# Kernel optimization log

Measured on AMD Instinct MI355X. Metric: run time of the kernel, lower is better.

The kernel has to match this reference:

```python
import jax, jax.numpy as jnp
import numpy as np

N_NODES = 10000
N_EDGES = 320000
IN_DIM = 64
HIDDEN = 128
HEADS = 4
OUT_DIM = 64
NEG_SLOPE = 0.2  # PyG GATConv default leaky_relu slope


def setup_inputs() -> dict:
    key = jax.random.key(0)
    ks = jax.random.split(key, 20)
    s = 0.05
    inp = {
        "x": jax.random.normal(ks[0], (N_NODES, IN_DIM), jnp.float32),
        "edge_index": jax.random.randint(ks[1], (2, N_EDGES), 0, N_NODES, jnp.int64),
        # GRU layer 0 (input IN_DIM -> HIDDEN), gates ordered [r, z, n] as in torch
        "w_ih0": jax.random.normal(ks[2], (3 * HIDDEN, IN_DIM), jnp.float32) * s,
        "w_hh0": jax.random.normal(ks[3], (3 * HIDDEN, HIDDEN), jnp.float32) * s,
        "b_ih0": jax.random.normal(ks[4], (3 * HIDDEN,), jnp.float32) * s,
        "b_hh0": jax.random.normal(ks[5], (3 * HIDDEN,), jnp.float32) * s,
        # GRU layer 1 (HIDDEN -> HIDDEN)
        "w_ih1": jax.random.normal(ks[6], (3 * HIDDEN, HIDDEN), jnp.float32) * s,
        "w_hh1": jax.random.normal(ks[7], (3 * HIDDEN, HIDDEN), jnp.float32) * s,
        "b_ih1": jax.random.normal(ks[8], (3 * HIDDEN,), jnp.float32) * s,
        "b_hh1": jax.random.normal(ks[9], (3 * HIDDEN,), jnp.float32) * s,
        # GAT layer 1: HIDDEN -> HIDDEN per head, HEADS heads, concat
        "W1": jax.random.normal(ks[10], (HIDDEN, HEADS * HIDDEN), jnp.float32) * s,
        "att_src1": jax.random.normal(ks[11], (HEADS, HIDDEN), jnp.float32) * s,
        "att_dst1": jax.random.normal(ks[12], (HEADS, HIDDEN), jnp.float32) * s,
        "bias1": jnp.zeros((HEADS * HIDDEN,), jnp.float32),
        # GAT layer 2: HEADS*HIDDEN -> OUT_DIM, 1 head
        "W2": jax.random.normal(ks[13], (HEADS * HIDDEN, OUT_DIM), jnp.float32) * s,
        "att_src2": jax.random.normal(ks[14], (1, OUT_DIM), jnp.float32) * s,
        "att_dst2": jax.random.normal(ks[15], (1, OUT_DIM), jnp.float32) * s,
        "bias2": jnp.zeros((OUT_DIM,), jnp.float32),
    }
    return inp


def _gru_layer(x, w_ih, w_hh, b_ih, b_hh):
    # x: [T, in]; torch GRU cell, unbatched, gates [r, z, n]
    H = w_hh.shape[1]
    gi = x @ w_ih.T + b_ih  # [T, 3H] precomputed input projections

    def step(h, gi_t):
        gh = h @ w_hh.T + b_hh
        i_r, i_z, i_n = jnp.split(gi_t, 3)
        h_r, h_z, h_n = jnp.split(gh, 3)
        r = jax.nn.sigmoid(i_r + h_r)
        z = jax.nn.sigmoid(i_z + h_z)
        n = jnp.tanh(i_n + r * h_n)
        h_new = (1.0 - z) * n + z * h
        return h_new, h_new

    h0 = jnp.zeros((H,), x.dtype)
    _, out = jax.lax.scan(step, h0, gi)
    return out  # [T, H]


def _gat(x, src, dst, W, att_src, att_dst, bias):
    # PyG GATConv (eval mode, add_self_loops=True, concat=True)
    N = x.shape[0]
    heads, C = att_src.shape
    h = (x @ W).reshape(N, heads, C)  # [N, H, C]
    loop = jnp.arange(N, dtype=src.dtype)
    s = jnp.concatenate([src, loop])
    d = jnp.concatenate([dst, loop])
    a_s = jnp.einsum("nhc,hc->nh", h, att_src)  # [N, H]
    a_d = jnp.einsum("nhc,hc->nh", h, att_dst)
    e = jax.nn.leaky_relu(a_s[s] + a_d[d], NEG_SLOPE)  # [E, H]
    m = jax.ops.segment_max(e, d, num_segments=N)  # per-dst max (every node has self loop)
    ex = jnp.exp(e - m[d])
    denom = jax.ops.segment_sum(ex, d, num_segments=N)
    alpha = ex / denom[d]  # [E, H]
    out = jax.ops.segment_sum(alpha[:, :, None] * h[s], d, num_segments=N)  # [N, H, C]
    return out.reshape(N, heads * C) + bias


def reference(x, edge_index,
              w_ih0, w_hh0, b_ih0, b_hh0,
              w_ih1, w_hh1, b_ih1, b_hh1,
              W1, att_src1, att_dst1, bias1,
              W2, att_src2, att_dst2, bias2):
    h = _gru_layer(x, w_ih0, w_hh0, b_ih0, b_hh0)
    h = _gru_layer(h, w_ih1, w_hh1, b_ih1, b_hh1)
    src, dst = edge_index[0], edge_index[1]
    h = _gat(h, src, dst, W1, att_src1, att_dst1, bias1)
    h = jax.nn.relu(h)
    out = _gat(h, src, dst, W2, att_src2, att_dst2, bias2)
    return out  # [N, OUT_DIM]
```

## Files before the change

kernel.cpp:

```cpp
#include <hip/hip_runtime.h>
#include <math.h>

#define NN_  10000
#define NE_  320000
#define IND  64
#define HID  128
#define G3   384
#define HC1  512
#define OUTD 64

typedef _Float16 h2f __attribute__((ext_vector_type(2)));
union UH4 { uint4 u; h2f h[4]; };

__device__ __forceinline__ float leakyf_(float x){ return x>0.f ? x : 0.2f*x; }
__device__ __forceinline__ float fsig_(float x){ return 1.f/(1.f+__expf(-x)); }
__device__ __forceinline__ float ftanh_(float x){ float e=__expf(2.f*x); return 1.f-2.f/(e+1.f); }

#define BARRIER_LDS() asm volatile("s_waitcnt lgkmcnt(0)\n\ts_barrier" ::: "memory")
#define WAIT_VM0()    asm volatile("s_waitcnt vmcnt(0)" ::: "memory")

__device__ __forceinline__ float ld_agent(const float* p) {
  return __hip_atomic_load(p, __ATOMIC_RELAXED, __HIP_MEMORY_SCOPE_AGENT);
}
__device__ __forceinline__ void st_agent(float* p, float v) {
  __hip_atomic_store(p, v, __ATOMIC_RELAXED, __HIP_MEMORY_SCOPE_AGENT);
}
__device__ __forceinline__ unsigned ld_agent_u32(const unsigned* p) {
  return __hip_atomic_load(p, __ATOMIC_RELAXED, __HIP_MEMORY_SCOPE_AGENT);
}
__device__ __forceinline__ void st_agent_u32(unsigned* p, unsigned v) {
  __hip_atomic_store(p, v, __ATOMIC_RELAXED, __HIP_MEMORY_SCOPE_AGENT);
}
__device__ __forceinline__ int ld_ctr(const int* p) {
  return __hip_atomic_load(p, __ATOMIC_ACQUIRE, __HIP_MEMORY_SCOPE_AGENT);
}
__device__ __forceinline__ void st_ctr(int* p, int v) {
  __hip_atomic_store(p, v, __ATOMIC_RELEASE, __HIP_MEMORY_SCOPE_AGENT);
}

template<bool TB>
__global__ __launch_bounds__(256) void gemm_k(const float* __restrict__ A,
                                              const float* __restrict__ B,
                                              const float* __restrict__ bias,
                                              float* __restrict__ C,
                                              int M, int N, int K) {
  __shared__ float As[16][65];
  __shared__ float Bs[16][65];
  const int bm = blockIdx.x * 64, bn = blockIdx.y * 64;
  const int tid = threadIdx.x;
  const int tm = (tid >> 4) << 2, tn = (tid & 15) << 2;
  float acc[4][4] = {};
  const int row = tid & 63, kq = (tid >> 6) << 2;
  for (int k0 = 0; k0 < K; k0 += 16) {
    float4 av = make_float4(0.f, 0.f, 0.f, 0.f);
    const int m = bm + row;
    if (m < M) av = *(const float4*)(A + (size_t)m * K + k0 + kq);
    As[kq + 0][row] = av.x; As[kq + 1][row] = av.y;
    As[kq + 2][row] = av.z; As[kq + 3][row] = av.w;
    if (TB) {
      float4 bv = *(const float4*)(B + (size_t)(bn + row) * K + k0 + kq);
      Bs[kq + 0][row] = bv.x; Bs[kq + 1][row] = bv.y;
      Bs[kq + 2][row] = bv.z; Bs[kq + 3][row] = bv.w;
    } else {
      const int kr = tid >> 4, nq = (tid & 15) << 2;
      float4 bv = *(const float4*)(B + (size_t)(k0 + kr) * N + bn + nq);
      Bs[kr][nq + 0] = bv.x; Bs[kr][nq + 1] = bv.y;
      Bs[kr][nq + 2] = bv.z; Bs[kr][nq + 3] = bv.w;
    }
    __syncthreads();
#pragma unroll
    for (int kk = 0; kk < 16; kk++) {
      float a[4], b[4];
#pragma unroll
      for (int i = 0; i < 4; i++) a[i] = As[kk][tm + i];
#pragma unroll
      for (int j = 0; j < 4; j++) b[j] = Bs[kk][tn + j];
#pragma unroll
      for (int i = 0; i < 4; i++)
#pragma unroll
        for (int j = 0; j < 4; j++) acc[i][j] = fmaf(a[i], b[j], acc[i][j]);
    }
    __syncthreads();
  }
#pragma unroll
  for (int i = 0; i < 4; i++) {
    const int m = bm + tm + i;
    if (m < M) {
#pragma unroll
      for (int j = 0; j < 4; j++) {
        const int n = bn + tn + j;
        float v = acc[i][j];
        if (bias) v += bias[n];
        C[(size_t)m * N + n] = v;
      }
    }
  }
}

__global__ __launch_bounds__(256, 1) void gru_pipe(const float* __restrict__ gi0,
                                                   const float* __restrict__ w_hh0,
                                                   const float* __restrict__ b_hh0,
                                                   const float* __restrict__ w_ih1,
                                                   const float* __restrict__ b_ih1,
                                                   const float* __restrict__ w_hh1,
                                                   const float* __restrict__ b_hh1,
                                                   unsigned* h0_st16, float* gi1_st,
                                                   int* ctr,
                                                   float* __restrict__ h1_out,
                                                   int T) {
  __shared__ _Float16 hbuf[2][HID];
  __shared__ float psum[3][HID];

  const int bid   = blockIdx.x;
  const int tid   = threadIdx.x;
  const int khalf = (tid >> 6) & 1;
  const int j     = (tid & 63) | ((tid >> 7) << 6);
  const int kbase = khalf * 64;

  const float* wsrc = (bid == 0) ? w_hh0 : (bid == 3 ? w_hh1 : w_ih1);
  const float* bsrc = (bid == 0) ? b_hh0 : (bid == 3 ? b_hh1 : b_ih1);

  h2f wr[32], wz[32], wn[32];
#pragma unroll
  for (int i = 0; i < 16; i++) {
    float4 a = *(const float4*)(wsrc + (size_t)j * HID + kbase + i * 4);
    wr[2 * i]     = h2f{(_Float16)a.x, (_Float16)a.y};
    wr[2 * i + 1] = h2f{(_Float16)a.z, (_Float16)a.w};
  }
#pragma unroll
  for (int i = 0; i < 16; i++) {
    float4 a = *(const float4*)(wsrc + (size_t)(j + HID) * HID + kbase + i * 4);
    wz[2 * i]     = h2f{(_Float16)a.x, (_Float16)a.y};
    wz[2 * i + 1] = h2f{(_Float16)a.z, (_Float16)a.w};
  }
#pragma unroll
  for (int i = 0; i < 16; i++) {
    float4 a = *(const float4*)(wsrc + (size_t)(j + 2 * HID) * HID + kbase + i * 4);
    wn[2 * i]     = h2f{(_Float16)a.x, (_Float16)a.y};
    wn[2 * i + 1] = h2f{(_Float16)a.z, (_Float16)a.w};
  }
  const float b0 = bsrc[j];
  const float b1 = bsrc[j + HID];
  const float b2 = bsrc[j + 2 * HID];

  auto dot_half = [&](const _Float16* hp16, float& r, float& z, float& n) {
    const uint4* hp = (const uint4*)(hp16 + kbase);
    float ar0 = 0.f, ar1 = 0.f, az0 = 0.f, az1 = 0.f, an0 = 0.f, an1 = 0.f;
#pragma unroll
    for (int c = 0; c < 2; c++) {
      uint4 hv[4];
#pragma unroll
      for (int i = 0; i < 4; i++) hv[i] = hp[c * 4 + i];
#pragma unroll
      for (int i = 0; i < 4; i++) {
        UH4 v; v.u = hv[i];
#pragma unroll
        for (int q = 0; q < 4; q++) {
          const int k = c * 16 + i * 4 + q;
          const h2f hh = v.h[q];
          if (k & 1) {
            ar1 = __builtin_amdgcn_fdot2(wr[k], hh, ar1, false);
            az1 = __builtin_amdgcn_fdot2(wz[k], hh, az1, false);
            an1 = __builtin_amdgcn_fdot2(wn[k], hh, an1, false);
          } else {
            ar0 = __builtin_amdgcn_fdot2(wr[k], hh, ar0, false);
            az0 = __builtin_amdgcn_fdot2(wz[k], hh, az0, false);
            an0 = __builtin_amdgcn_fdot2(wn[k], hh, an0, false);
          }
        }
      }
    }
    r = ar0 + ar1; z = az0 + az1; n = an0 + an1;
  };

  if (bid == 0 || bid == 3) {
    const float* gsrc = (bid == 0) ? gi0 : gi1_st;
    float hcur = 0.f;
    if (khalf == 0) hbuf[0][j] = (_Float16)0.f;
    BARRIER_LDS();

    if (bid == 3 && tid == 0) {
      while (ld_ctr(&ctr[1]) < 4) {}
      while (ld_ctr(&ctr[2]) < 4) {}
    }
    if (bid == 3) __syncthreads();

    float gxA, gyA, gzA, gxB, gyB, gzB, gxC, gyC, gzC, gxD, gyD, gzD;
    if (khalf == 0) {
      const float* gp = gsrc + j;
      gxA = gp[0]; gyA = gp[HID]; gzA = gp[2 * HID];
      gp = gsrc + (size_t)1 * G3 + j;
      gxB = gp[0]; gyB = gp[HID]; gzB = gp[2 * HID];
      gp = gsrc + (size_t)2 * G3 + j;
      gxC = gp[0]; gyC = gp[HID]; gzC = gp[2 * HID];
      gp = gsrc + (size_t)3 * G3 + j;
      gxD = gp[0]; gyD = gp[HID]; gzD = gp[2 * HID];
    }

    auto substep = [&](int tc, int pin, float& gx, float& gy, float& gz) {
      float dr, dz, dn;
      dot_half(&hbuf[pin][0], dr, dz, dn);
      if (khalf == 1) { psum[0][j] = dr; psum[1][j] = dz; psum[2][j] = dn; }
      BARRIER_LDS();
      if (khalf == 0) {
        const float r = fsig_(gx + b0 + dr + psum[0][j]);
        const float z = fsig_(gy + b1 + dz + psum[1][j]);
        const float n = ftanh_(gz + r * (b2 + dn + psum[2][j]));
        hcur = (1.f - z) * n + z * hcur;
        hbuf[pin ^ 1][j] = (_Float16)hcur;
        if (bid == 3) h1_out[(size_t)tc * HID + j] = hcur;
        const int tp = (tc + 4 < T) ? (tc + 4) : 0;
        const float* gp = gsrc + (size_t)tp * G3 + j;
        gx = gp[0]; gy = gp[HID]; gz = gp[2 * HID];
      }
      if (bid == 3 && tid == 0 && (tc & 31) == 0) {
        int need = tc + 36; if (need > T) need = T;
        while (ld_ctr(&ctr[1]) < need) {}
        while (ld_ctr(&ctr[2]) < need) {}
      }
      BARRIER_LDS();
      if (bid == 0 && tid >= 64 && tid < 128) {
        const int idx = tid - 64;
        unsigned v = *(const unsigned*)&hbuf[pin ^ 1][2 * idx];
        st_agent_u32(&h0_st16[(size_t)tc * 64 + idx], v);
        if ((tc & 7) == 7) {
          WAIT_VM0();
          if (tid == 64) st_ctr(&ctr[0], tc + 1);
        }
      }
    };

    for (int t = 0; t < T; t += 4) {
      substep(t,     0, gxA, gyA, gzA);
      substep(t + 1, 1, gxB, gyB, gzB);
      substep(t + 2, 0, gxC, gyC, gzC);
      substep(t + 3, 1, gxD, gyD, gzD);
    }
    if (bid == 0 && tid >= 64 && tid < 128) {
      WAIT_VM0();
      if (tid == 64) st_ctr(&ctr[0], T);
    }
  } else {
    const int f = bid - 1;
    _Float16* hstage = &hbuf[0][0];
    for (int t0 = f; t0 < T; t0 += 8) {
      if (tid == 0) {
        int need = t0 + 7; if (need > T) need = T;
        while (ld_ctr(&ctr[0]) < need) {}
      }
      __syncthreads();
      unsigned hv0 = 0, hv1 = 0, hv2 = 0, hv3 = 0;
      if (tid < 64) {
        hv0 = ld_agent_u32(&h0_st16[(size_t)t0 * 64 + tid]);
        if (t0 + 2 < T) hv1 = ld_agent_u32(&h0_st16[(size_t)(t0 + 2) * 64 + tid]);
        if (t0 + 4 < T) hv2 = ld_agent_u32(&h0_st16[(size_t)(t0 + 4) * 64 + tid]);
        if (t0 + 6 < T) hv3 = ld_agent_u32(&h0_st16[(size_t)(t0 + 6) * 64 + tid]);
      }
#pragma unroll
      for (int k = 0; k < 4; k++) {
        const int t = t0 + 2 * k;
        if (t >= T) break;
        if (tid < 64) {
          const unsigned hv = (k == 0) ? hv0 : (k == 1) ? hv1 : (k == 2) ? hv2 : hv3;
          ((unsigned*)hstage)[tid] = hv;
        }
        BARRIER_LDS();
        float dr, dz, dn;
        dot_half(hstage, dr, dz, dn);
        if (khalf == 1) { psum[0][j] = dr; psum[1][j] = dz; psum[2][j] = dn; }
        BARRIER_LDS();
        if (khalf == 0) {
          float* gp = gi1_st + (size_t)t * G3 + j;
          st_agent(gp,           dr + psum[0][j] + b0);
          st_agent(gp + HID,     dz + psum[1][j] + b1);
          st_agent(gp + 2 * HID, dn + psum[2][j] + b2);
        }
      }
      __syncthreads();
      if (tid == 0) {
        int pub = t0 + 8; if (pub > T) pub = T;
        st_ctr(&ctr[1 + f], pub);
      }
    }
    __syncthreads();
    if (tid == 0) st_ctr(&ctr[1 + f], T);
  }
}

__global__ void att_dots(const float* __restrict__ feat,
                         const float* __restrict__ att_src,
                         const float* __restrict__ att_dst,
                         float* __restrict__ a_s, float* __restrict__ a_d,
                         int heads, int C) {
  const int n = blockIdx.x;
  const int h = threadIdx.x >> 6;
  const int lane = threadIdx.x & 63;
  float ss = 0.f, dd = 0.f;
  const float* f = feat + (size_t)n * heads * C + h * C;
  for (int c = lane; c < C; c += 64) {
    const float v = f[c];
    ss = fmaf(v, att_src[h * C + c], ss);
    dd = fmaf(v, att_dst[h * C + c], dd);
  }
#pragma unroll
  for (int o = 32; o > 0; o >>= 1) {
    ss += __shfl_down(ss, o);
    dd += __shfl_down(dd, o);
  }
  if (lane == 0) { a_s[n * heads + h] = ss; a_d[n * heads + h] = dd; }
}

__global__ void edge_count(const int* __restrict__ ei, int* __restrict__ cnt, int E) {
  const int e = blockIdx.x * 256 + threadIdx.x;
  if (e < E) atomicAdd(&cnt[ei[E + e]], 1);
}

__global__ __launch_bounds__(1024) void prefix_scan(const int* __restrict__ cnt,
                                                    int* __restrict__ offs,
                                                    int* __restrict__ cursor, int N) {
  __shared__ int buf[1024];
  __shared__ int carry;
  const int tid = threadIdx.x;
  if (tid == 0) carry = 0;
  __syncthreads();
  for (int base = 0; base < N; base += 1024) {
    const int i = base + tid;
    const int v = (i < N) ? cnt[i] : 0;
    buf[tid] = v;
    __syncthreads();
    for (int d = 1; d < 1024; d <<= 1) {
      int t = 0;
      if (tid >= d) t = buf[tid - d];
      __syncthreads();
      buf[tid] += t;
      __syncthreads();
    }
    const int incl = buf[tid] + carry;
    if (i < N) { offs[i] = incl - v; cursor[i] = incl - v; }
    __syncthreads();
    if (tid == 1023) carry = incl;
    __syncthreads();
  }
  if (tid == 0) offs[N] = carry;
}

__global__ void edge_fill(const int* __restrict__ ei, int* __restrict__ cursor,
                          int* __restrict__ csr, int E) {
  const int e = blockIdx.x * 256 + threadIdx.x;
  if (e < E) {
    const int d = ei[E + e];
    const int s = ei[e];
    const int pos = atomicAdd(&cursor[d], 1);
    csr[pos] = s;
  }
}

__global__ void gat_agg(const float* __restrict__ feat,
                        const float* __restrict__ a_s, const float* __restrict__ a_d,
                        const int* __restrict__ offs, const int* __restrict__ csr,
                        const float* __restrict__ bias, float* __restrict__ out,
                        int heads, int cshift, int do_relu) {
  const int n = blockIdx.x;
  const int t = threadIdx.x;
  const int HC = blockDim.x;
  const int h = t >> cshift;
  const int beg = offs[n], end = offs[n + 1];
  const float ad = a_d[n * heads + h];
  const float self_e = leakyf_(a_s[n * heads + h] + ad);
  float m = self_e;
  for (int i = beg; i < end; i++) {
    const int s = csr[i];
    m = fmaxf(m, leakyf_(a_s[s * heads + h] + ad));
  }
  float den = expf(self_e - m);
  float acc = den * feat[(size_t)n * HC + t];
  for (int i = beg; i < end; i++) {
    const int s = csr[i];
    const float wgt = expf(leakyf_(a_s[s * heads + h] + ad) - m);
    den += wgt;
    acc = fmaf(wgt, feat[(size_t)s * HC + t], acc);
  }
  float o = acc / den + bias[t];
  if (do_relu) o = fmaxf(o, 0.f);
  out[(size_t)n * HC + t] = o;
}

extern "C" void kernel_launch(void* const* d_in, const int* in_sizes, int n_in,
                              void* d_out, int out_size, void* d_ws, size_t ws_size,
                              hipStream_t stream) {
  const float* x        = (const float*)d_in[0];
  const int*   ei       = (const int*)d_in[1];
  const float* w_ih0    = (const float*)d_in[2];
  const float* w_hh0    = (const float*)d_in[3];
  const float* b_ih0    = (const float*)d_in[4];
  const float* b_hh0    = (const float*)d_in[5];
  const float* w_ih1    = (const float*)d_in[6];
  const float* w_hh1    = (const float*)d_in[7];
  const float* b_ih1    = (const float*)d_in[8];
  const float* b_hh1    = (const float*)d_in[9];
  const float* W1       = (const float*)d_in[10];
  const float* att_src1 = (const float*)d_in[11];
  const float* att_dst1 = (const float*)d_in[12];
  const float* bias1    = (const float*)d_in[13];
  const float* W2       = (const float*)d_in[14];
  const float* att_src2 = (const float*)d_in[15];
  const float* att_dst2 = (const float*)d_in[16];
  const float* bias2    = (const float*)d_in[17];
  float* out = (float*)d_out;

  const int N = NN_;
  const int E = in_sizes[1] / 2;

  float* f    = (float*)d_ws;
  float* gi   = f;
  float* hmm1 = f;
  float* h1   = f + (size_t)N * HC1;
  float* g1o  = h1 + (size_t)N * HID;
  float* hmm2 = g1o + (size_t)N * HC1;
  float* as1  = hmm2 + (size_t)N * OUTD;
  float* ad1  = as1 + (size_t)N * 4;
  float* as2  = ad1 + (size_t)N * 4;
  float* ad2  = as2 + (size_t)N;
  int* cnt    = (int*)(ad2 + (size_t)N);
  int* offs   = cnt + N;
  int* cursor = offs + (N + 1);
  int* csr    = cursor + N;
  int* ctr    = csr + E;
  unsigned* h0_st16 = (unsigned*)g1o;
  float*    gi1_st  = g1o + (size_t)N * 64;

  const int mblocks = (N + 63) / 64;

  gemm_k<true><<<dim3(mblocks, G3 / 64), 256, 0, stream>>>(x, w_ih0, b_ih0, gi, N, G3, IND);
  hipMemsetAsync(ctr, 0, 3 * sizeof(int), stream);
  gru_pipe<<<4, 256, 0, stream>>>(gi, w_hh0, b_hh0, w_ih1, b_ih1, w_hh1, b_hh1,
                                  h0_st16, gi1_st, ctr, h1, N);

  hipMemsetAsync(cnt, 0, (size_t)N * sizeof(int), stream);
  edge_count<<<(E + 255) / 256, 256, 0, stream>>>(ei, cnt, E);
  prefix_scan<<<1, 1024, 0, stream>>>(cnt, offs, cursor, N);
  edge_fill<<<(E + 255) / 256, 256, 0, stream>>>(ei, cursor, csr, E);

  gemm_k<false><<<dim3(mblocks, HC1 / 64), 256, 0, stream>>>(h1, W1, nullptr, hmm1, N, HC1, HID);
  att_dots<<<N, 4 * 64, 0, stream>>>(hmm1, att_src1, att_dst1, as1, ad1, 4, HID);
  gat_agg<<<N, HC1, 0, stream>>>(hmm1, as1, ad1, offs, csr, bias1, g1o, 4, 7, 1);

  gemm_k<false><<<dim3(mblocks, OUTD / 64), 256, 0, stream>>>(g1o, W2, nullptr, hmm2, N, OUTD, HC1);
  att_dots<<<N, 1 * 64, 0, stream>>>(hmm2, att_src2, att_dst2, as2, ad2, 1, OUTD);
  gat_agg<<<N, OUTD, 0, stream>>>(hmm2, as2, ad2, offs, csr, bias2, out, 1, 6, 0);
}
```

Measured before the change: 6.313 ms.

## Overlap CSR construction with the GRU recurrence by adding side blocks to gru_pipe

Extra blocks are appended to the persistent GRU kernel so that the edge count, prefix scan and CSR fill run at the same time as the serial 4-block GRU recurrence, instead of as separate kernels launched after it. The side blocks coordinate through agent-scope counters in ctr[3] and ctr[4] using spin-waits, and the scan now runs in 256-thread chunks. This hides the CSR build latency behind the long sequential GRU. In exchange it relies on all blocks being co-resident to avoid deadlock, and it could contend with the GRU blocks for memory or atomics bandwidth.

```diff
diff --git a/kernel.cpp b/kernel.cpp
--- a/kernel.cpp
+++ b/kernel.cpp
@@ -8,6 +8,9 @@
 #define G3   384
 #define HC1  512
 #define OUTD 64
+
+#define CSR_CNT_BLKS 40
+#define CSR_FILL_BLKS 40
 
 typedef _Float16 h2f __attribute__((ext_vector_type(2)));
 union UH4 { uint4 u; h2f h[4]; };
@@ -107,12 +110,73 @@
                                                    unsigned* h0_st16, float* gi1_st,
                                                    int* ctr,
                                                    float* __restrict__ h1_out,
-                                                   int T) {
+                                                   int T,
+                                                   const int* __restrict__ ei,
+                                                   int* cnt, int* offs,
+                                                   int* cursor, int* csr, int E) {
   __shared__ _Float16 hbuf[2][HID];
   __shared__ float psum[3][HID];
+  __shared__ int sbuf[256];
+  __shared__ int scarry;
 
   const int bid   = blockIdx.x;
   const int tid   = threadIdx.x;
+
+  if (bid >= 4) {
+    const int cb = bid - 4;
+    if (cb < CSR_CNT_BLKS) {
+      for (int e = cb * 256 + tid; e < E; e += CSR_CNT_BLKS * 256)
+        atomicAdd(&cnt[ei[E + e]], 1);
+      __syncthreads();
+      if (tid == 0)
+        __hip_atomic_fetch_add(&ctr[3], 1, __ATOMIC_RELEASE, __HIP_MEMORY_SCOPE_AGENT);
+    } else if (cb == CSR_CNT_BLKS) {
+      if (tid == 0) {
+        while (ld_ctr(&ctr[3]) < CSR_CNT_BLKS) __builtin_amdgcn_s_sleep(32);
+      }
+      __syncthreads();
+      if (tid == 0) scarry = 0;
+      __syncthreads();
+      for (int base = 0; base < NN_; base += 256) {
+        const int i = base + tid;
+        const int v = (i < NN_) ? cnt[i] : 0;
+        sbuf[tid] = v;
+        __syncthreads();
+        for (int d = 1; d < 256; d <<= 1) {
+          int t2 = 0;
+          if (tid >= d) t2 = sbuf[tid - d];
+          __syncthreads();
+          sbuf[tid] += t2;
+          __syncthreads();
+        }
+        const int incl = sbuf[tid] + scarry;
+        if (i < NN_) { offs[i] = incl - v; cursor[i] = incl - v; }
+        __syncthreads();
+        if (tid == 255) scarry = incl;
+        __syncthreads();
+      }
+      if (tid == 0) {
+        offs[NN_] = scarry;
+        __threadfence();
+        st_ctr(&ctr[4], 1);
+      }
+    } else {
+      const int fb = cb - CSR_CNT_BLKS - 1;
+      if (tid == 0) {
+        while (ld_ctr(&ctr[4]) < 1) __builtin_amdgcn_s_sleep(64);
+      }
+      __syncthreads();
+      for (int e = fb * 256 + tid; e < E; e += CSR_FILL_BLKS * 256) {
+        const int d = ei[E + e];
+        const int s = ei[e];
+        const int pos = atomicAdd(&cursor[d], 1);
+        csr[pos] = s;
+      }
+    }
+    return;
+  }
+
+  const int lane  = tid & 63;
   const int khalf = (tid >> 6) & 1;
   const int j     = (tid & 63) | ((tid >> 7) << 6);
   const int kbase = khalf * 64;
@@ -308,51 +372,6 @@
     dd += __shfl_down(dd, o);
   }
   if (lane == 0) { a_s[n * heads + h] = ss; a_d[n * heads + h] = dd; }
-}
-
-__global__ void edge_count(const int* __restrict__ ei, int* __restrict__ cnt, int E) {
-  const int e = blockIdx.x * 256 + threadIdx.x;
-  if (e < E) atomicAdd(&cnt[ei[E + e]], 1);
-}
-
-__global__ __launch_bounds__(1024) void prefix_scan(const int* __restrict__ cnt,
-                                                    int* __restrict__ offs,
-                                                    int* __restrict__ cursor, int N) {
-  __shared__ int buf[1024];
-  __shared__ int carry;
-  const int tid = threadIdx.x;
-  if (tid == 0) carry = 0;
-  __syncthreads();
-  for (int base = 0; base < N; base += 1024) {
-    const int i = base + tid;
-    const int v = (i < N) ? cnt[i] : 0;
-    buf[tid] = v;
-    __syncthreads();
-    for (int d = 1; d < 1024; d <<= 1) {
-      int t = 0;
-      if (tid >= d) t = buf[tid - d];
-      __syncthreads();
-      buf[tid] += t;
-      __syncthreads();
-    }
-    const int incl = buf[tid] + carry;
-    if (i < N) { offs[i] = incl - v; cursor[i] = incl - v; }
-    __syncthreads();
-    if (tid == 1023) carry = incl;
-    __syncthreads();
-  }
-  if (tid == 0) offs[N] = carry;
-}
-
-__global__ void edge_fill(const int* __restrict__ ei, int* __restrict__ cursor,
-                          int* __restrict__ csr, int E) {
-  const int e = blockIdx.x * 256 + threadIdx.x;
-  if (e < E) {
-    const int d = ei[E + e];
-    const int s = ei[e];
-    const int pos = atomicAdd(&cursor[d], 1);
-    csr[pos] = s;
-  }
 }
 
 __global__ void gat_agg(const float* __restrict__ feat,
@@ -432,14 +451,11 @@
   const int mblocks = (N + 63) / 64;
 
   gemm_k<true><<<dim3(mblocks, G3 / 64), 256, 0, stream>>>(x, w_ih0, b_ih0, gi, N, G3, IND);
-  hipMemsetAsync(ctr, 0, 3 * sizeof(int), stream);
-  gru_pipe<<<4, 256, 0, stream>>>(gi, w_hh0, b_hh0, w_ih1, b_ih1, w_hh1, b_hh1,
-                                  h0_st16, gi1_st, ctr, h1, N);
-
+  hipMemsetAsync(ctr, 0, 6 * sizeof(int), stream);
   hipMemsetAsync(cnt, 0, (size_t)N * sizeof(int), stream);
-  edge_count<<<(E + 255) / 256, 256, 0, stream>>>(ei, cnt, E);
-  prefix_scan<<<1, 1024, 0, stream>>>(cnt, offs, cursor, N);
-  edge_fill<<<(E + 255) / 256, 256, 0, stream>>>(ei, cursor, csr, E);
+  gru_pipe<<<4 + CSR_CNT_BLKS + 1 + CSR_FILL_BLKS, 256, 0, stream>>>(
+      gi, w_hh0, b_hh0, w_ih1, b_ih1, w_hh1, b_hh1,
+      h0_st16, gi1_st, ctr, h1, N, ei, cnt, offs, cursor, csr, E);
 
   gemm_k<false><<<dim3(mblocks, HC1 / 64), 256, 0, stream>>>(h1, W1, nullptr, hmm1, N, HC1, HID);
   att_dots<<<N, 4 * 64, 0, stream>>>(hmm1, att_src1, att_dst1, as1, ad1, 4, HID);
```

After: 6.295 ms. No clear change (-0.3%).
